# Performance work log

Measured on AMD Instinct MI355X. Metric: run time of the kernel, lower is better.

The kernel has to match this reference:

```python
import jax, jax.numpy as jnp
import numpy as np

GRID = 192
ISO = 0.0

CORNERS = [(0,0,0),(1,0,0),(0,1,0),(1,1,0),(0,0,1),(1,0,1),(0,1,1),(1,1,1)]
# 12 cube edges as pairs of corner offsets
EDGES = [
    ((0,0,0),(1,0,0)),((0,1,0),(1,1,0)),((0,0,1),(1,0,1)),((0,1,1),(1,1,1)),
    ((0,0,0),(0,1,0)),((1,0,0),(1,1,0)),((0,0,1),(0,1,1)),((1,0,1),(1,1,1)),
    ((0,0,0),(0,0,1)),((1,0,0),(1,0,1)),((0,1,0),(0,1,1)),((1,1,0),(1,1,1)),
]


def setup_inputs() -> dict:
    key = jax.random.key(0)
    grid = jax.random.normal(key, (GRID, GRID, GRID), dtype=jnp.float32)
    return {"grid": grid}


def _dual_verts(grid, iso):
    # One dual vertex per cell of the padded grid: mean of the iso-crossing
    # points on the cell's 12 edges (dual-marching-cubes vertex placement).
    X, Y, Z = grid.shape
    P = jnp.pad(grid, 1, constant_values=iso + 1.0)  # (X+2, Y+2, Z+2)
    Cx, Cy, Cz = X + 1, Y + 1, Z + 1                 # number of cells per axis
    vals = {c: P[c[0]:c[0]+Cx, c[1]:c[1]+Cy, c[2]:c[2]+Cz] for c in CORNERS}
    sum_pt = jnp.zeros((Cx, Cy, Cz, 3), grid.dtype)
    cnt = jnp.zeros((Cx, Cy, Cz), grid.dtype)
    for ca, cb in EDGES:  # fixed 12-iteration loop, fully vectorized over cells
        vA, vB = vals[ca], vals[cb]
        m = (vA < iso) != (vB < iso)                 # edge crosses isosurface
        t = jnp.where(m, (iso - vA) / jnp.where(m, vB - vA, 1.0), 0.0)
        oa = jnp.asarray(ca, grid.dtype)
        ob = jnp.asarray(cb, grid.dtype)
        pt = oa + t[..., None] * (ob - oa)           # local crossing point
        mf = m.astype(grid.dtype)
        sum_pt = sum_pt + mf[..., None] * pt
        cnt = cnt + mf
    base = jnp.stack(jnp.meshgrid(jnp.arange(Cx), jnp.arange(Cy), jnp.arange(Cz), indexing='ij'), axis=-1).astype(grid.dtype)
    verts = base + sum_pt / jnp.maximum(cnt, 1.0)[..., None]
    # undo +1 padding offset, then normalize by (dim - 1) as in the module
    verts = (verts - 1.0) / (jnp.asarray([X, Y, Z], grid.dtype) - 1.0)
    return verts.reshape(-1, 3), (cnt > 0).reshape(-1)


def _quads(grid, iso):
    # One quad per grid edge that crosses the isosurface, connecting the dual
    # vertices of the 4 cells sharing that edge. Emitted densely with a mask
    # (jit-compatible fixed shapes); masked rows are inactive.
    X, Y, Z = grid.shape
    P = jnp.pad(grid, 1, constant_values=iso + 1.0)
    Cx, Cy, Cz = X + 1, Y + 1, Z + 1
    sgn = P < iso
    def cid(a, b, c):  # flatten cell index
        return (a * Cy + b) * Cz + c
    qs, ms = [], []
    # x-directed edges: shared by cells (i, j-1/j, k-1/k)
    m = sgn[0:Cx, 1:Cy, 1:Cz] != sgn[1:Cx+1, 1:Cy, 1:Cz]
    a = jnp.arange(Cx)[:, None, None]; b = jnp.arange(1, Cy)[None, :, None]; c = jnp.arange(1, Cz)[None, None, :]
    q = jnp.stack(jnp.broadcast_arrays(cid(a, b-1, c-1), cid(a, b, c-1), cid(a, b, c), cid(a, b-1, c)), axis=-1)
    qs.append(q.reshape(-1, 4)); ms.append(m.reshape(-1))
    # y-directed edges: shared by cells (i-1/i, j, k-1/k)
    m = sgn[1:Cx, 0:Cy, 1:Cz] != sgn[1:Cx, 1:Cy+1, 1:Cz]
    a = jnp.arange(1, Cx)[:, None, None]; b = jnp.arange(Cy)[None, :, None]; c = jnp.arange(1, Cz)[None, None, :]
    q = jnp.stack(jnp.broadcast_arrays(cid(a-1, b, c-1), cid(a, b, c-1), cid(a, b, c), cid(a-1, b, c)), axis=-1)
    qs.append(q.reshape(-1, 4)); ms.append(m.reshape(-1))
    # z-directed edges: shared by cells (i-1/i, j-1/j, k)
    m = sgn[1:Cx, 1:Cy, 0:Cz] != sgn[1:Cx, 1:Cy, 1:Cz+1]
    a = jnp.arange(1, Cx)[:, None, None]; b = jnp.arange(1, Cy)[None, :, None]; c = jnp.arange(Cz)[None, None, :]
    q = jnp.stack(jnp.broadcast_arrays(cid(a-1, b-1, c), cid(a, b-1, c), cid(a, b, c), cid(a-1, b, c)), axis=-1)
    qs.append(q.reshape(-1, 4)); ms.append(m.reshape(-1))
    quads = jnp.concatenate(qs, axis=0).astype(jnp.int32)
    qmask = jnp.concatenate(ms, axis=0)
    return quads, qmask


def reference(grid):
    verts, vmask = _dual_verts(grid, ISO)
    quads, qmask = _quads(grid, ISO)
    return verts, vmask, quads, qmask
```

## Files before the change

### kernel.cpp

```cpp
#include <hip/hip_runtime.h>

#define GN 192
#define CN 193

#define NV        ((size_t)CN * CN * CN)
#define OFF_VMASK ((size_t)(NV * 3))
#define OFF_QUADS ((size_t)(OFF_VMASK + NV))
#define QSEG      ((size_t)CN * GN * GN)
#define OFF_QMASK ((size_t)(OFF_QUADS + 3 * QSEG * 4))

__device__ __forceinline__ float gpad(const float* __restrict__ g, int x, int y, int z) {
    if ((unsigned)x < (unsigned)GN && (unsigned)y < (unsigned)GN && (unsigned)z < (unsigned)GN)
        return g[((size_t)x * GN + y) * GN + z];
    return 1.0f;
}

__device__ __forceinline__ bool spad(const float* __restrict__ g, int px, int py, int pz) {
    int x = px - 1, y = py - 1, z = pz - 1;
    if ((unsigned)x < (unsigned)GN && (unsigned)y < (unsigned)GN && (unsigned)z < (unsigned)GN)
        return g[((size_t)x * GN + y) * GN + z] < 0.0f;
    return false;
}

__device__ __forceinline__ float fcid(int a, int b, int c) {
    return (float)((a * CN + b) * CN + c);
}

__global__ __launch_bounds__(256) void verts_kernel(const float* __restrict__ g,
                                                    float* __restrict__ out) {
    const int k = threadIdx.x;
    const int j = blockIdx.y;
    const int i = blockIdx.z;
    if (k >= CN) return;

    const float v000 = gpad(g, i - 1, j - 1, k - 1);
    const float v100 = gpad(g, i,     j - 1, k - 1);
    const float v010 = gpad(g, i - 1, j,     k - 1);
    const float v110 = gpad(g, i,     j,     k - 1);
    const float v001 = gpad(g, i - 1, j - 1, k);
    const float v101 = gpad(g, i,     j - 1, k);
    const float v011 = gpad(g, i - 1, j,     k);
    const float v111 = gpad(g, i,     j,     k);

    float sx = 0.f, sy = 0.f, sz = 0.f;
    int cnt = 0;

    auto acc = [&](float vA, float vB, int axis, float o1, float o2) {
        if ((vA < 0.f) != (vB < 0.f)) {
            float t = -vA / (vB - vA);
            if (axis == 0)      { sx += t;  sy += o1; sz += o2; }
            else if (axis == 1) { sx += o1; sy += t;  sz += o2; }
            else                { sx += o1; sy += o2; sz += t;  }
            cnt++;
        }
    };
    acc(v000, v100, 0, 0.f, 0.f);
    acc(v010, v110, 0, 1.f, 0.f);
    acc(v001, v101, 0, 0.f, 1.f);
    acc(v011, v111, 0, 1.f, 1.f);
    acc(v000, v010, 1, 0.f, 0.f);
    acc(v100, v110, 1, 1.f, 0.f);
    acc(v001, v011, 1, 0.f, 1.f);
    acc(v101, v111, 1, 1.f, 1.f);
    acc(v000, v001, 2, 0.f, 0.f);
    acc(v100, v101, 2, 1.f, 0.f);
    acc(v010, v011, 2, 0.f, 1.f);
    acc(v110, v111, 2, 1.f, 1.f);

    const float cm = fmaxf((float)cnt, 1.0f);
    const float inv191 = 1.0f / 191.0f;
    const float vx = ((float)i + sx / cm - 1.0f) * inv191;
    const float vy = ((float)j + sy / cm - 1.0f) * inv191;
    const float vz = ((float)k + sz / cm - 1.0f) * inv191;

    const size_t idx = ((size_t)i * CN + j) * CN + k;
    out[idx * 3 + 0] = vx;
    out[idx * 3 + 1] = vy;
    out[idx * 3 + 2] = vz;
    out[OFF_VMASK + idx] = (cnt > 0) ? 1.0f : 0.0f;
}

__global__ __launch_bounds__(256) void quadsA(const float* __restrict__ g,
                                              float* __restrict__ out) {
    const int t = blockIdx.x * 256 + threadIdx.x;
    const int a = blockIdx.z;
    const int bi = t / GN, ci = t % GN;

    const bool m = spad(g, a, bi + 1, ci + 1) != spad(g, a + 1, bi + 1, ci + 1);
    const size_t r = ((size_t)a * GN + bi) * GN + ci;

    float4 q;
    q.x = fcid(a, bi,     ci);
    q.y = fcid(a, bi + 1, ci);
    q.z = fcid(a, bi + 1, ci + 1);
    q.w = fcid(a, bi,     ci + 1);
    ((float4*)(out + OFF_QUADS))[r] = q;
    out[OFF_QMASK + r] = m ? 1.0f : 0.0f;
}

__global__ __launch_bounds__(256) void quadsB(const float* __restrict__ g,
                                              float* __restrict__ out) {
    const int t = blockIdx.x * 256 + threadIdx.x;
    if (t >= CN * GN) return;
    const int a = blockIdx.z + 1;
    const int b = t / GN, ci = t % GN;

    const bool m = spad(g, a, b, ci + 1) != spad(g, a, b + 1, ci + 1);
    const size_t r = QSEG + ((size_t)(a - 1) * CN + b) * GN + ci;

    float4 q;
    q.x = fcid(a - 1, b, ci);
    q.y = fcid(a,     b, ci);
    q.z = fcid(a,     b, ci + 1);
    q.w = fcid(a - 1, b, ci + 1);
    ((float4*)(out + OFF_QUADS))[r] = q;
    out[OFF_QMASK + r] = m ? 1.0f : 0.0f;
}

__global__ __launch_bounds__(256) void quadsC(const float* __restrict__ g,
                                              float* __restrict__ out) {
    const int t = blockIdx.x * 256 + threadIdx.x;
    if (t >= GN * CN) return;
    const int a = blockIdx.z + 1;
    const int bi = t / CN, c = t % CN;
    const int b = bi + 1;

    const bool m = spad(g, a, b, c) != spad(g, a, b, c + 1);
    const size_t r = 2 * QSEG + ((size_t)bi * CN + c) + (size_t)(a - 1) * GN * CN;

    float4 q;
    q.x = fcid(a - 1, b - 1, c);
    q.y = fcid(a,     b - 1, c);
    q.z = fcid(a,     b,     c);
    q.w = fcid(a - 1, b,     c);
    ((float4*)(out + OFF_QUADS))[r] = q;
    out[OFF_QMASK + r] = m ? 1.0f : 0.0f;
}

extern "C" void kernel_launch(void* const* d_in, const int* in_sizes, int n_in,
                              void* d_out, int out_size, void* d_ws, size_t ws_size,
                              hipStream_t stream) {
    const float* g = (const float*)d_in[0];
    float* out = (float*)d_out;

    verts_kernel<<<dim3(1, CN, CN), dim3(256), 0, stream>>>(g, out);

    quadsA<<<dim3(144, 1, CN), dim3(256), 0, stream>>>(g, out);
    quadsB<<<dim3(145, 1, GN), dim3(256), 0, stream>>>(g, out);
    quadsC<<<dim3(145, 1, GN), dim3(256), 0, stream>>>(g, out);
}
```

Baseline: 598.6 us.

## Fuse vertex and quad kernels into one dense per-cell launch

```diff
diff --git a/kernel.cpp b/kernel.cpp
--- a/kernel.cpp
+++ b/kernel.cpp
@@ -2,6 +2,7 @@
 
 #define GN 192
 #define CN 193
+#define CN2 (CN * CN)
 
 #define NV        ((size_t)CN * CN * CN)
 #define OFF_VMASK ((size_t)(NV * 3))
@@ -15,23 +16,15 @@
     return 1.0f;
 }
 
-__device__ __forceinline__ bool spad(const float* __restrict__ g, int px, int py, int pz) {
-    int x = px - 1, y = py - 1, z = pz - 1;
-    if ((unsigned)x < (unsigned)GN && (unsigned)y < (unsigned)GN && (unsigned)z < (unsigned)GN)
-        return g[((size_t)x * GN + y) * GN + z] < 0.0f;
-    return false;
-}
-
-__device__ __forceinline__ float fcid(int a, int b, int c) {
-    return (float)((a * CN + b) * CN + c);
-}
-
-__global__ __launch_bounds__(256) void verts_kernel(const float* __restrict__ g,
-                                                    float* __restrict__ out) {
-    const int k = threadIdx.x;
-    const int j = blockIdx.y;
-    const int i = blockIdx.z;
-    if (k >= CN) return;
+__global__ __launch_bounds__(256) void dmc_fused(const float* __restrict__ g,
+                                                 float* __restrict__ out) {
+    const size_t lin = (size_t)blockIdx.x * 256 + threadIdx.x;
+    if (lin >= NV) return;
+    const int linI = (int)lin;
+    const int k = linI % CN;
+    const int t2 = linI / CN;
+    const int j = t2 % CN;
+    const int i = t2 / CN;
 
     const float v000 = gpad(g, i - 1, j - 1, k - 1);
     const float v100 = gpad(g, i,     j - 1, k - 1);
@@ -42,99 +35,74 @@
     const float v011 = gpad(g, i - 1, j,     k);
     const float v111 = gpad(g, i,     j,     k);
 
+    const bool s000 = v000 < 0.f, s100 = v100 < 0.f, s010 = v010 < 0.f, s110 = v110 < 0.f;
+    const bool s001 = v001 < 0.f, s101 = v101 < 0.f, s011 = v011 < 0.f, s111 = v111 < 0.f;
+
     float sx = 0.f, sy = 0.f, sz = 0.f;
     int cnt = 0;
-
-    auto acc = [&](float vA, float vB, int axis, float o1, float o2) {
-        if ((vA < 0.f) != (vB < 0.f)) {
-            float t = -vA / (vB - vA);
+    auto acc = [&](float vA, float vB, bool sA, bool sB, int axis, float o1, float o2) {
+        if (sA != sB) {
+            const float t = -vA * __builtin_amdgcn_rcpf(vB - vA);
             if (axis == 0)      { sx += t;  sy += o1; sz += o2; }
             else if (axis == 1) { sx += o1; sy += t;  sz += o2; }
             else                { sx += o1; sy += o2; sz += t;  }
             cnt++;
         }
     };
-    acc(v000, v100, 0, 0.f, 0.f);
-    acc(v010, v110, 0, 1.f, 0.f);
-    acc(v001, v101, 0, 0.f, 1.f);
-    acc(v011, v111, 0, 1.f, 1.f);
-    acc(v000, v010, 1, 0.f, 0.f);
-    acc(v100, v110, 1, 1.f, 0.f);
-    acc(v001, v011, 1, 0.f, 1.f);
-    acc(v101, v111, 1, 1.f, 1.f);
-    acc(v000, v001, 2, 0.f, 0.f);
-    acc(v100, v101, 2, 1.f, 0.f);
-    acc(v010, v011, 2, 0.f, 1.f);
-    acc(v110, v111, 2, 1.f, 1.f);
+    acc(v000, v100, s000, s100, 0, 0.f, 0.f);
+    acc(v010, v110, s010, s110, 0, 1.f, 0.f);
+    acc(v001, v101, s001, s101, 0, 0.f, 1.f);
+    acc(v011, v111, s011, s111, 0, 1.f, 1.f);
+    acc(v000, v010, s000, s010, 1, 0.f, 0.f);
+    acc(v100, v110, s100, s110, 1, 1.f, 0.f);
+    acc(v001, v011, s001, s011, 1, 0.f, 1.f);
+    acc(v101, v111, s101, s111, 1, 1.f, 1.f);
+    acc(v000, v001, s000, s001, 2, 0.f, 0.f);
+    acc(v100, v101, s100, s101, 2, 1.f, 0.f);
+    acc(v010, v011, s010, s011, 2, 0.f, 1.f);
+    acc(v110, v111, s110, s111, 2, 1.f, 1.f);
 
-    const float cm = fmaxf((float)cnt, 1.0f);
+    const float rc = __builtin_amdgcn_rcpf(fmaxf((float)cnt, 1.0f));
     const float inv191 = 1.0f / 191.0f;
-    const float vx = ((float)i + sx / cm - 1.0f) * inv191;
-    const float vy = ((float)j + sy / cm - 1.0f) * inv191;
-    const float vz = ((float)k + sz / cm - 1.0f) * inv191;
+    out[lin * 3 + 0] = ((float)i + sx * rc - 1.0f) * inv191;
+    out[lin * 3 + 1] = ((float)j + sy * rc - 1.0f) * inv191;
+    out[lin * 3 + 2] = ((float)k + sz * rc - 1.0f) * inv191;
+    out[OFF_VMASK + lin] = (cnt > 0) ? 1.0f : 0.0f;
 
-    const size_t idx = ((size_t)i * CN + j) * CN + k;
-    out[idx * 3 + 0] = vx;
-    out[idx * 3 + 1] = vy;
-    out[idx * 3 + 2] = vz;
-    out[OFF_VMASK + idx] = (cnt > 0) ? 1.0f : 0.0f;
-}
+    const float flin = (float)linI;
+    float4* const quads = (float4*)(out + OFF_QUADS);
+    float* const qmask = out + OFF_QMASK;
 
-__global__ __launch_bounds__(256) void quadsA(const float* __restrict__ g,
-                                              float* __restrict__ out) {
-    const int t = blockIdx.x * 256 + threadIdx.x;
-    const int a = blockIdx.z;
-    const int bi = t / GN, ci = t % GN;
-
-    const bool m = spad(g, a, bi + 1, ci + 1) != spad(g, a + 1, bi + 1, ci + 1);
-    const size_t r = ((size_t)a * GN + bi) * GN + ci;
-
-    float4 q;
-    q.x = fcid(a, bi,     ci);
-    q.y = fcid(a, bi + 1, ci);
-    q.z = fcid(a, bi + 1, ci + 1);
-    q.w = fcid(a, bi,     ci + 1);
-    ((float4*)(out + OFF_QUADS))[r] = q;
-    out[OFF_QMASK + r] = m ? 1.0f : 0.0f;
-}
-
-__global__ __launch_bounds__(256) void quadsB(const float* __restrict__ g,
-                                              float* __restrict__ out) {
-    const int t = blockIdx.x * 256 + threadIdx.x;
-    if (t >= CN * GN) return;
-    const int a = blockIdx.z + 1;
-    const int b = t / GN, ci = t % GN;
-
-    const bool m = spad(g, a, b, ci + 1) != spad(g, a, b + 1, ci + 1);
-    const size_t r = QSEG + ((size_t)(a - 1) * CN + b) * GN + ci;
-
-    float4 q;
-    q.x = fcid(a - 1, b, ci);
-    q.y = fcid(a,     b, ci);
-    q.z = fcid(a,     b, ci + 1);
-    q.w = fcid(a - 1, b, ci + 1);
-    ((float4*)(out + OFF_QUADS))[r] = q;
-    out[OFF_QMASK + r] = m ? 1.0f : 0.0f;
-}
-
-__global__ __launch_bounds__(256) void quadsC(const float* __restrict__ g,
-                                              float* __restrict__ out) {
-    const int t = blockIdx.x * 256 + threadIdx.x;
-    if (t >= GN * CN) return;
-    const int a = blockIdx.z + 1;
-    const int bi = t / CN, c = t % CN;
-    const int b = bi + 1;
-
-    const bool m = spad(g, a, b, c) != spad(g, a, b, c + 1);
-    const size_t r = 2 * QSEG + ((size_t)bi * CN + c) + (size_t)(a - 1) * GN * CN;
-
-    float4 q;
-    q.x = fcid(a - 1, b - 1, c);
-    q.y = fcid(a,     b - 1, c);
-    q.z = fcid(a,     b,     c);
-    q.w = fcid(a - 1, b,     c);
-    ((float4*)(out + OFF_QUADS))[r] = q;
-    out[OFF_QMASK + r] = m ? 1.0f : 0.0f;
+    if (j < GN && k < GN) {
+        const size_t r = ((size_t)i * GN + j) * GN + k;
+        float4 q;
+        q.x = flin;
+        q.y = flin + (float)CN;
+        q.z = flin + (float)(CN+1);
+        q.w = flin + 1.0f;
+        quads[r] = q;
+        qmask[r] = (s011 != s111) ? 1.0f : 0.0f;
+    }
+    if (i >= 1 && k < GN) {
+        const size_t r = QSEG + ((size_t)(i - 1) * CN + j) * GN + k;
+        float4 q;
+        q.x = flin - (float)CN2;
+        q.y = flin;
+        q.z = flin + 1.0f;
+        q.w = flin - (float)(CN2 - 1);
+        quads[r] = q;
+        qmask[r] = (s001 != s011) ? 1.0f : 0.0f;
+    }
+    if (i >= 1 && j >= 1) {
+        const size_t r = 2 * QSEG + ((size_t)(i - 1) * GN + (j - 1)) * CN + k;
+        float4 q;
+        q.x = flin - (float)(CN2 + CN);
+        q.y = flin - (float)CN;
+        q.z = flin;
+        q.w = flin - (float)CN2;
+        quads[r] = q;
+        qmask[r] = (s000 != s001) ? 1.0f : 0.0f;
+    }
 }
 
 extern "C" void kernel_launch(void* const* d_in, const int* in_sizes, int n_in,
@@ -142,10 +110,6 @@
                               hipStream_t stream) {
     const float* g = (const float*)d_in[0];
     float* out = (float*)d_out;
-
-    verts_kernel<<<dim3(1, CN, CN), dim3(256), 0, stream>>>(g, out);
-
-    quadsA<<<dim3(144, 1, CN), dim3(256), 0, stream>>>(g, out);
-    quadsB<<<dim3(145, 1, GN), dim3(256), 0, stream>>>(g, out);
-    quadsC<<<dim3(145, 1, GN), dim3(256), 0, stream>>>(g, out);
+    const int nblocks = (int)((NV + 255) / 256);
+    dmc_fused<<<dim3(nblocks), dim3(256), 0, stream>>>(g, out);
 }
```

Result: faster. 557.3 us (-6.9%).
